# Optimization experiments

Measured on AMD Instinct MI355X. Metric: run time of the kernel, lower is better.

The kernel has to match this reference:

```python
import jax, jax.numpy as jnp
import numpy as np

DIM = 512
HEADS = 8
R = 8  # reduction_ratio
EPS = 1e-08


def setup_inputs() -> dict:
    key = jax.random.key(0)
    k1, k2, k3, k4, k5 = jax.random.split(key, 5)
    B, H, W = 2, 128, 128
    x = jax.random.normal(k1, (B, DIM, H, W), dtype=jnp.float32)
    mask = jax.random.uniform(k2, (B, 1, H, W), dtype=jnp.float32)
    # learned params (conv weights, OIHW)
    Wq = jax.random.normal(k3, (DIM, DIM, 1, 1), dtype=jnp.float32) * 0.02
    Wkv = jax.random.normal(k4, (2 * DIM, DIM, R, R), dtype=jnp.float32) * 0.02
    Wo = jax.random.normal(k5, (DIM, DIM, 1, 1), dtype=jnp.float32) * 0.02
    return {"x": x, "mask": mask, "Wq": Wq, "Wkv": Wkv, "Wo": Wo}


def reference(x, mask, Wq, Wkv, Wo):
    B, C, H, W = x.shape
    heads = HEADS
    hd = C // heads  # head dim
    scale = hd ** (-0.5)
    N = H * W
    Hr, Wr = H // R, W // R
    L = Hr * Wr

    # to_q: 1x1 conv (no bias)
    q = jnp.einsum('bchw,oc->bohw', x, Wq[:, :, 0, 0])
    # to_kv: conv kernel R stride R (no bias)
    kv = jax.lax.conv_general_dilated(
        x, Wkv, window_strides=(R, R), padding='VALID',
        dimension_numbers=('NCHW', 'OIHW', 'NCHW'))
    k, v = jnp.split(kv, 2, axis=1)  # each [B, C, Hr, Wr]

    # nn.Unfold(R, stride=R) on [B,1,H,W] then mean over patch dim == avg-pool R/R
    mask_down = mask.reshape(B, Hr, R, Wr, R).mean(axis=(2, 4)).reshape(B, L)  # [B, L]
    m_flat = mask.reshape(B, N)  # [B, N]  (c == 1)
    # rank-1 outer-product bias, then log
    bias = jnp.log(m_flat[:, :, None] * mask_down[:, None, :] + EPS)  # [B, N, L]

    def to_tokens(t, n):
        # 'b (h c) x y -> (b h) (x y) c'
        Bt = t.shape[0]
        return t.reshape(Bt, heads, hd, n).transpose(0, 1, 3, 2).reshape(Bt * heads, n, hd)

    qh = to_tokens(q, N)   # [B*heads, N, hd]
    kh = to_tokens(k, L)   # [B*heads, L, hd]
    vh = to_tokens(v, L)   # [B*heads, L, hd]

    # torch mask.repeat(heads,1,1): tiles whole [B,...] block heads times -> index i uses bias[i % B]
    bias_rep = jnp.tile(bias, (heads, 1, 1))  # [heads*B, N, L]

    sim = (jnp.einsum('bic,bjc->bij', qh, kh) + bias_rep) * scale
    attn = jax.nn.softmax(sim, axis=-1)
    out = jnp.einsum('bij,bjc->bic', attn, vh)  # [B*heads, N, hd]

    # '(b h) (x y) c -> b (h c) x y'
    out = out.reshape(B, heads, N, hd).transpose(0, 1, 3, 2).reshape(B, C, H, W)
    return jnp.einsum('bchw,oc->bohw', out, Wo[:, :, 0, 0])
```

## Files before the change

kernel.cpp:

```cpp
#include <hip/hip_runtime.h>
#include <math.h>

#define DIMC  512
#define HEADS 8
#define HD    64
#define NPIX  16384
#define LTOK  256
#define BATCH 2
#define WIMG  128
#define KVK   32768
#define EPSB  1e-8f
#define SCALEF 0.125f
#define SPLITK 16
#define KCHUNK (KVK / SPLITK)

typedef unsigned short ushort_t;
typedef unsigned int uint_t;
using bf16x8 = __attribute__((ext_vector_type(8))) __bf16;
using f32x4  = __attribute__((ext_vector_type(4))) float;

__device__ __forceinline__ ushort_t f2bf(float f) {
    union { float f; unsigned u; } v; v.f = f;
    unsigned r = v.u + 0x7FFFu + ((v.u >> 16) & 1u);
    return (ushort_t)(r >> 16);
}
__device__ __forceinline__ float bf2f(ushort_t h) {
    union { unsigned u; float f; } v; v.u = ((unsigned)h) << 16;
    return v.f;
}
__device__ __forceinline__ uint_t pk2bf(float a, float b) {
    return (uint_t)f2bf(a) | ((uint_t)f2bf(b) << 16);
}
__device__ __forceinline__ void gl16(const void* g, void* l) {
    __builtin_amdgcn_global_load_lds(
        (const __attribute__((address_space(1))) unsigned int*)g,
        (__attribute__((address_space(3))) unsigned int*)l, 16, 0, 0);
}

__global__ void k_maskdown(const float* __restrict__ mask, float* __restrict__ md) {
    int b = blockIdx.x;
    int l = threadIdx.x;
    int hr = l >> 4, wr = l & 15;
    const float* mp = mask + (size_t)b * NPIX;
    float s = 0.f;
#pragma unroll
    for (int i = 0; i < 8; ++i)
#pragma unroll
        for (int j = 0; j < 8; ++j)
            s += mp[(hr * 8 + i) * WIMG + wr * 8 + j];
    md[b * LTOK + l] = s * (1.f / 64.f);
}

__global__ __launch_bounds__(256) void k_xt(const float* __restrict__ x, ushort_t* __restrict__ xt) {
    __shared__ float t[64][65];
    int b = blockIdx.z, c0 = blockIdx.y * 64, n0 = blockIdx.x * 64;
    int tn = threadIdx.x & 63, tc = threadIdx.x >> 6;
    const float* xb = x + ((size_t)b * DIMC + c0) * NPIX + n0;
#pragma unroll
    for (int p = 0; p < 16; ++p)
        t[tc + p * 4][tn] = xb[(size_t)(tc + p * 4) * NPIX + tn];
    __syncthreads();
    ushort_t* xtb = xt + ((size_t)b * NPIX + n0) * DIMC + c0;
#pragma unroll
    for (int p = 0; p < 16; ++p) {
        int nl = tc + p * 4;
        xtb[(size_t)nl * DIMC + tn] = f2bf(t[tn][nl]);
    }
}

__global__ __launch_bounds__(256) void k_wkvp(const float* __restrict__ Wkv, ushort_t* __restrict__ Wp) {
    __shared__ float t[64][65];
    int o = blockIdx.y, c0 = blockIdx.x * 64;
    int tij = threadIdx.x & 63, tc = threadIdx.x >> 6;
    const float* wb = Wkv + ((size_t)o * DIMC + c0) * 64;
#pragma unroll
    for (int p = 0; p < 16; ++p)
        t[tc + p * 4][tij] = wb[(size_t)(tc + p * 4) * 64 + tij];
    __syncthreads();
    ushort_t* wpb = Wp + (size_t)o * KVK + c0;
#pragma unroll
    for (int p = 0; p < 16; ++p) {
        int ij = tc + p * 4;
        wpb[(size_t)ij * DIMC + tij] = f2bf(t[tij][ij]);
    }
}

__global__ void k_cvt(const float* __restrict__ s, ushort_t* __restrict__ d) {
    int i = blockIdx.x * 256 + threadIdx.x;
    d[i] = f2bf(s[i]);
}

template<int EPI>
__global__ __launch_bounds__(256) void k_gemm_qo(
    const ushort_t* __restrict__ A, long sA,
    const ushort_t* __restrict__ B, long sB,
    void* __restrict__ Yv) {
    __shared__ ushort_t Asm[2][128 * 64];
    __shared__ ushort_t Bsm[2][128 * 64];
    const int tid = threadIdx.x;
    const int w = tid >> 6, lane = tid & 63;
    const int wm = w >> 1, wn = w & 1;
    const int lr = lane & 15, lg = lane >> 4;
    const int bz = blockIdx.z;
    const int m0 = blockIdx.y * 128, c0 = blockIdx.x * 128;
    const ushort_t* Ab = A + (size_t)bz * sA;
    const ushort_t* Bb = B + (size_t)bz * sB;

    f32x4 acc[4][4];
    const f32x4 zz = {0.f, 0.f, 0.f, 0.f};
#pragma unroll
    for (int i = 0; i < 4; ++i)
#pragma unroll
        for (int j = 0; j < 4; ++j) acc[i][j] = zz;

#define STAGE_QO(buf, k0) do {                                               \
    _Pragma("unroll")                                                        \
    for (int r = 0; r < 4; ++r) {                                            \
        int slot = r * 256 + tid;                                            \
        int m = slot >> 3, kb = slot & 7;                                    \
        int kbs = kb ^ (m & 7);                                              \
        gl16(Ab + (size_t)(m0 + m) * DIMC + (k0) + kbs * 8,                  \
             &Asm[buf][(size_t)(r * 256 + w * 64) * 8]);                     \
    }                                                                        \
    _Pragma("unroll")                                                        \
    for (int r = 0; r < 4; ++r) {                                            \
        int slot = r * 256 + tid;                                            \
        int m = slot >> 3, kb = slot & 7;                                    \
        int kbs = kb ^ (m & 7);                                              \
        gl16(Bb + (size_t)(c0 + m) * DIMC + (k0) + kbs * 8,                  \
             &Bsm[buf][(size_t)(r * 256 + w * 64) * 8]);                     \
    }                                                                        \
} while (0)

    STAGE_QO(0, 0);
    __syncthreads();
    int cur = 0;
#pragma unroll 1
    for (int t = 0; t < 8; ++t) {
        if (t < 7) STAGE_QO(cur ^ 1, (t + 1) * 64);
#pragma unroll
        for (int kk = 0; kk < 2; ++kk) {
            bf16x8 af[4], bfr[4];
#pragma unroll
            for (int i = 0; i < 4; ++i) {
                int row = wm * 64 + i * 16 + lr;
                af[i] = *(const bf16x8*)&Asm[cur][(size_t)(row * 8 + ((kk * 4 + lg) ^ (row & 7))) * 8];
            }
#pragma unroll
            for (int j = 0; j < 4; ++j) {
                int row = wn * 64 + j * 16 + lr;
                bfr[j] = *(const bf16x8*)&Bsm[cur][(size_t)(row * 8 + ((kk * 4 + lg) ^ (row & 7))) * 8];
            }
#pragma unroll
            for (int i = 0; i < 4; ++i)
#pragma unroll
                for (int j = 0; j < 4; ++j)
                    acc[i][j] = __builtin_amdgcn_mfma_f32_16x16x32_bf16(af[i], bfr[j], acc[i][j], 0, 0, 0);
        }
        if (t < 7) {
            __syncthreads();
            cur ^= 1;
        }
    }
#undef STAGE_QO

    if (EPI == 0) {
        ushort_t* q = (ushort_t*)Yv + (size_t)bz * ((size_t)NPIX * DIMC);
#pragma unroll
        for (int i = 0; i < 4; ++i) {
            int d0 = m0 + wm * 64 + i * 16 + lg * 4;
#pragma unroll
            for (int j = 0; j < 4; ++j) {
                int n = c0 + wn * 64 + j * 16 + lr;
                ushort4 v;
                v.x = f2bf(acc[i][j][0]); v.y = f2bf(acc[i][j][1]);
                v.z = f2bf(acc[i][j][2]); v.w = f2bf(acc[i][j][3]);
                *(ushort4*)&q[(size_t)n * DIMC + d0] = v;
            }
        }
    } else {
        float* O = (float*)Yv + (size_t)bz * ((size_t)DIMC * NPIX);
#pragma unroll
        for (int i = 0; i < 4; ++i) {
            int n0r = m0 + wm * 64 + i * 16 + lg * 4;
#pragma unroll
            for (int j = 0; j < 4; ++j) {
                int o = c0 + wn * 64 + j * 16 + lr;
                *(f32x4*)&O[(size_t)o * NPIX + n0r] = acc[i][j];
            }
        }
    }
}

__global__ __launch_bounds__(256) void k_convkv_mfma(
    const ushort_t* __restrict__ xt, const ushort_t* __restrict__ Wp,
    float* __restrict__ part) {
    __shared__ ushort_t Asm[2][128 * 64];
    __shared__ ushort_t Bsm[2][128 * 64];
    const int tid = threadIdx.x;
    const int w = tid >> 6, lane = tid & 63;
    const int wm = w >> 1, wn = w & 1;
    const int lr = lane & 15, lg = lane >> 4;
    const int z = blockIdx.z;
    const int b = z >> 4, ks = z & 15;
    const int m0 = blockIdx.y * 128, n0 = blockIdx.x * 128;
    const ushort_t* xtb = xt + (size_t)b * NPIX * DIMC;
    const int kbeg = ks * KCHUNK;

    f32x4 acc[4][4];
    const f32x4 zz = {0.f, 0.f, 0.f, 0.f};
#pragma unroll
    for (int i = 0; i < 4; ++i)
#pragma unroll
        for (int j = 0; j < 4; ++j) acc[i][j] = zz;

#define STAGE_KV(buf, k0) do {                                               \
    _Pragma("unroll")                                                        \
    for (int r = 0; r < 4; ++r) {                                            \
        int slot = r * 256 + tid;                                            \
        int m = slot >> 3, kb = slot & 7;                                    \
        int kbs = kb ^ (m & 7);                                              \
        gl16(Wp + (size_t)(m0 + m) * KVK + (k0) + kbs * 8,                   \
             &Asm[buf][(size_t)(r * 256 + w * 64) * 8]);                     \
    }                                                                        \
    _Pragma("unroll")                                                        \
    for (int r = 0; r < 4; ++r) {                                            \
        int slot = r * 256 + tid;                                            \
        int nn = slot >> 3, kb = slot & 7;                                   \
        int l = n0 + nn, hr = l >> 4, wr = l & 15;                           \
        int kp = (k0) + (kb ^ (nn & 7)) * 8;                                 \
        int ij = kp >> 9, ck = kp & 511;                                     \
        int ii = ij >> 3, jj = ij & 7;                                       \
        gl16(xtb + (size_t)((hr * 8 + ii) * WIMG + wr * 8 + jj) * DIMC + ck, \
             &Bsm[buf][(size_t)(r * 256 + w * 64) * 8]);                     \
    }                                                                        \
} while (0)

    STAGE_KV(0, kbeg);
    __syncthreads();
    int cur = 0;
#pragma unroll 1
    for (int t = 0; t < KCHUNK / 64; ++t) {
        if (t < KCHUNK / 64 - 1) STAGE_KV(cur ^ 1, kbeg + (t + 1) * 64);
#pragma unroll
        for (int kk = 0; kk < 2; ++kk) {
            bf16x8 af[4], bfr[4];
#pragma unroll
            for (int i = 0; i < 4; ++i) {
                int row = wm * 64 + i * 16 + lr;
                af[i] = *(const bf16x8*)&Asm[cur][(size_t)(row * 8 + ((kk * 4 + lg) ^ (row & 7))) * 8];
            }
#pragma unroll
            for (int j = 0; j < 4; ++j) {
                int row = wn * 64 + j * 16 + lr;
                bfr[j] = *(const bf16x8*)&Bsm[cur][(size_t)(row * 8 + ((kk * 4 + lg) ^ (row & 7))) * 8];
            }
#pragma unroll
            for (int i = 0; i < 4; ++i)
#pragma unroll
                for (int j = 0; j < 4; ++j)
                    acc[i][j] = __builtin_amdgcn_mfma_f32_16x16x32_bf16(af[i], bfr[j], acc[i][j], 0, 0, 0);
        }
        if (t < KCHUNK / 64 - 1) {
            __syncthreads();
            cur ^= 1;
        }
    }
#undef STAGE_KV

    float* P = part + (size_t)z * (LTOK * 1024);
#pragma unroll
    for (int i = 0; i < 4; ++i) {
        int o0 = m0 + wm * 64 + i * 16 + lg * 4;
#pragma unroll
        for (int j = 0; j < 4; ++j) {
            int l = n0 + wn * 64 + j * 16 + lr;
            *(f32x4*)&P[(size_t)l * 1024 + o0] = acc[i][j];
        }
    }
}

__global__ void k_kvreduce(const float* __restrict__ part,
                           ushort_t* __restrict__ kt, ushort_t* __restrict__ vt) {
    int idx = blockIdx.x * 256 + threadIdx.x;
    int o = idx & 1023;
    int rest = idx >> 10;
    int l = rest & 255, b = rest >> 8;
    float s = 0.f;
#pragma unroll
    for (int ks = 0; ks < SPLITK; ++ks)
        s += part[(size_t)(b * SPLITK + ks) * (LTOK * 1024) + (size_t)l * 1024 + o];
    int h = (o >> 6) & 7, d = o & 63;
    if (o < 512)
        kt[(((size_t)b * 8 + h) * 256 + l) * 64 + d] = f2bf(s);
    else
        vt[(((size_t)b * 8 + h) * 64 + d) * 256 + l] = f2bf(s);
}

__global__ __launch_bounds__(256, 2) void k_attn_mfma(
    const ushort_t* __restrict__ qbf, const ushort_t* __restrict__ kt,
    const ushort_t* __restrict__ vt, const float* __restrict__ mask,
    const float* __restrict__ md, ushort_t* __restrict__ obuf) {
    __shared__ ushort_t Qs[128 * 64];
    __shared__ ushort_t Ks[256 * 64];
    __shared__ ushort_t Vs[64 * 256];

    const int tid = threadIdx.x;
    const int w = tid >> 6, lane = tid & 63;
    const int g = lane >> 4, ln = lane & 15;
    const int bh = blockIdx.y, b = bh >> 3, h = bh & 7;
    const int bb = bh & 1;
    const int n0 = blockIdx.x * 128;

    {
        const ushort_t* src = qbf + ((size_t)b * NPIX + n0) * DIMC + h * 64;
#pragma unroll
        for (int p = 0; p < 4; ++p) {
            int id = p * 256 + tid;
            int r = id >> 3, s = id & 7;
            uint4 v = *(const uint4*)(src + (size_t)r * DIMC + s * 8);
            *(uint4*)&Qs[(r * 8 + (s ^ (r & 7))) * 8] = v;
        }
    }
    {
        const ushort_t* src = kt + (size_t)bh * 256 * 64;
#pragma unroll
        for (int p = 0; p < 8; ++p) {
            int id = p * 256 + tid;
            int r = id >> 3, s = id & 7;
            uint4 v = *(const uint4*)(src + r * 64 + s * 8);
            *(uint4*)&Ks[(r * 8 + (s ^ (r & 7))) * 8] = v;
        }
    }
    {
        const ushort_t* src = vt + (size_t)bh * 64 * 256;
#pragma unroll
        for (int p = 0; p < 8; ++p) {
            int id = p * 256 + tid;
            int r = id >> 5, s = id & 31;
            uint4 v = *(const uint4*)(src + r * 256 + s * 8);
            *(uint4*)&Vs[(r * 32 + (s ^ (r & 7))) * 8] = v;
        }
    }
    __syncthreads();

    f32x4 acc[2][16];
    const f32x4 zz = {0.f, 0.f, 0.f, 0.f};
#pragma unroll
    for (int nf = 0; nf < 2; ++nf)
#pragma unroll
        for (int f = 0; f < 16; ++f) acc[nf][f] = zz;

    bf16x8 qf[2][2];
#pragma unroll
    for (int nf = 0; nf < 2; ++nf)
#pragma unroll
        for (int kk = 0; kk < 2; ++kk) {
            int nl = 32 * w + nf * 16 + ln;
            qf[nf][kk] = *(const bf16x8*)&Qs[(nl * 8 + ((kk * 4 + g) ^ (nl & 7))) * 8];
        }
#pragma unroll
    for (int f = 0; f < 16; ++f) {
#pragma unroll
        for (int kk = 0; kk < 2; ++kk) {
            int l = f * 16 + ln;
            bf16x8 kf = *(const bf16x8*)&Ks[(l * 8 + ((kk * 4 + g) ^ (l & 7))) * 8];
            acc[0][f] = __builtin_amdgcn_mfma_f32_16x16x32_bf16(kf, qf[0][kk], acc[0][f], 0, 0, 0);
            acc[1][f] = __builtin_amdgcn_mfma_f32_16x16x32_bf16(kf, qf[1][kk], acc[1][f], 0, 0, 0);
        }
    }

    float inv[2];
    uint2 pb[2][16];
#pragma unroll
    for (int nf = 0; nf < 2; ++nf) {
        float mval = mask[(size_t)bb * NPIX + n0 + 32 * w + nf * 16 + ln];
        float mx = -1e30f;
#pragma unroll
        for (int f = 0; f < 16; ++f) {
            float4 md4 = *(const float4*)&md[bb * LTOK + f * 16 + g * 4];
            float s0 = (acc[nf][f][0] + __logf(mval * md4.x + EPSB)) * SCALEF;
            float s1 = (acc[nf][f][1] + __logf(mval * md4.y + EPSB)) * SCALEF;
            float s2 = (acc[nf][f][2] + __logf(mval * md4.z + EPSB)) * SCALEF;
            float s3 = (acc[nf][f][3] + __logf(mval * md4.w + EPSB)) * SCALEF;
            acc[nf][f][0] = s0; acc[nf][f][1] = s1;
            acc[nf][f][2] = s2; acc[nf][f][3] = s3;
            mx = fmaxf(mx, fmaxf(fmaxf(s0, s1), fmaxf(s2, s3)));
        }
        mx = fmaxf(mx, __shfl_xor(mx, 16));
        mx = fmaxf(mx, __shfl_xor(mx, 32));
        float sum = 0.f;
#pragma unroll
        for (int f = 0; f < 16; ++f) {
            float p0 = __expf(acc[nf][f][0] - mx);
            float p1 = __expf(acc[nf][f][1] - mx);
            float p2 = __expf(acc[nf][f][2] - mx);
            float p3 = __expf(acc[nf][f][3] - mx);
            sum += (p0 + p1) + (p2 + p3);
            pb[nf][f].x = pk2bf(p0, p1);
            pb[nf][f].y = pk2bf(p2, p3);
        }
        sum += __shfl_xor(sum, 16);
        sum += __shfl_xor(sum, 32);
        inv[nf] = 1.f / sum;
    }

    f32x4 acc2[2][4];
#pragma unroll
    for (int nf = 0; nf < 2; ++nf)
#pragma unroll
        for (int df = 0; df < 4; ++df) acc2[nf][df] = zz;

    const int srcLo = ((g & 1) << 5) + ln;
    const bool selHi = (g >> 1);
#pragma unroll
    for (int ks = 0; ks < 8; ++ks) {
        bf16x8 vf[4];
#pragma unroll
        for (int df = 0; df < 4; ++df) {
            int d = df * 16 + ln;
            vf[df] = *(const bf16x8*)&Vs[(d * 32 + ((ks * 4 + g) ^ (d & 7))) * 8];
        }
#pragma unroll
        for (int nf = 0; nf < 2; ++nf) {
            uint_t e0 = pb[nf][2 * ks].x,     e1 = pb[nf][2 * ks].y;
            uint_t o0 = pb[nf][2 * ks + 1].x, o1 = pb[nf][2 * ks + 1].y;
            uint_t lo0 = __shfl((int)e0, srcLo), lo1 = __shfl((int)e1, srcLo);
            uint_t lo0b = __shfl((int)o0, srcLo), lo1b = __shfl((int)o1, srcLo);
            uint_t hi0 = __shfl((int)e0, srcLo + 16), hi1 = __shfl((int)e1, srcLo + 16);
            uint_t hi0b = __shfl((int)o0, srcLo + 16), hi1b = __shfl((int)o1, srcLo + 16);
            union { uint_t u[4]; bf16x8 v; } bfr;
            bfr.u[0] = selHi ? lo0b : lo0;
            bfr.u[1] = selHi ? lo1b : lo1;
            bfr.u[2] = selHi ? hi0b : hi0;
            bfr.u[3] = selHi ? hi1b : hi1;
#pragma unroll
            for (int df = 0; df < 4; ++df)
                acc2[nf][df] = __builtin_amdgcn_mfma_f32_16x16x32_bf16(vf[df], bfr.v, acc2[nf][df], 0, 0, 0);
        }
    }

#pragma unroll
    for (int nf = 0; nf < 2; ++nf) {
        int n = n0 + 32 * w + nf * 16 + ln;
        ushort_t* op = obuf + ((size_t)b * NPIX + n) * DIMC + h * 64;
#pragma unroll
        for (int df = 0; df < 4; ++df) {
            ushort4 v;
            v.x = f2bf(acc2[nf][df][0] * inv[nf]);
            v.y = f2bf(acc2[nf][df][1] * inv[nf]);
            v.z = f2bf(acc2[nf][df][2] * inv[nf]);
            v.w = f2bf(acc2[nf][df][3] * inv[nf]);
            *(ushort4*)&op[df * 16 + g * 4] = v;
        }
    }
}

extern "C" void kernel_launch(void* const* d_in, const int* in_sizes, int n_in,
                              void* d_out, int out_size, void* d_ws, size_t ws_size,
                              hipStream_t stream) {
    const float* x    = (const float*)d_in[0];
    const float* mask = (const float*)d_in[1];
    const float* Wq   = (const float*)d_in[2];
    const float* Wkv  = (const float*)d_in[3];
    const float* Wo   = (const float*)d_in[4];
    float* out = (float*)d_out;

    char* ws = (char*)d_ws;
    float*    md   = (float*)(ws);
    ushort_t* xt   = (ushort_t*)(ws + 4096);
    ushort_t* wkvp = (ushort_t*)(ws + 33558528);
    ushort_t* qbf  = wkvp;
    ushort_t* ktb  = (ushort_t*)(ws + 100667392);
    ushort_t* vtb  = ktb + 524288;
    ushort_t* wqb  = (ushort_t*)(ws + 102764544);
    ushort_t* wob  = wqb + 262144;
    float*    part = (float*)(ws + 103813120);
    ushort_t* aob  = (ushort_t*)part;

    k_maskdown<<<dim3(BATCH), dim3(256), 0, stream>>>(mask, md);
    k_xt<<<dim3(NPIX / 64, DIMC / 64, BATCH), dim3(256), 0, stream>>>(x, xt);
    k_cvt<<<dim3(1024), dim3(256), 0, stream>>>(Wq, wqb);
    k_cvt<<<dim3(1024), dim3(256), 0, stream>>>(Wo, wob);
    k_wkvp<<<dim3(DIMC / 64, 1024), dim3(256), 0, stream>>>(Wkv, wkvp);

    k_convkv_mfma<<<dim3(LTOK / 128, 1024 / 128, BATCH * SPLITK), dim3(256), 0, stream>>>(xt, wkvp, part);
    k_kvreduce<<<dim3(2048), dim3(256), 0, stream>>>(part, ktb, vtb);

    k_gemm_qo<0><<<dim3(NPIX / 128, DIMC / 128, BATCH), dim3(256), 0, stream>>>(
        wqb, 0L, xt, (long)NPIX * DIMC, qbf);

    k_attn_mfma<<<dim3(NPIX / 128, BATCH * HEADS), dim3(256), 0, stream>>>(
        qbf, ktb, vtb, mask, md, aob);

    k_gemm_qo<1><<<dim3(DIMC / 128, NPIX / 128, BATCH), dim3(256), 0, stream>>>(
        aob, (long)NPIX * DIMC, wob, 0L, out);
}
```

Measured before the change: 248.3 us.

## Fuse Q projection into attention kernel and remap convkv blocks across XCDs

```diff
diff --git a/kernel.cpp b/kernel.cpp
--- a/kernel.cpp
+++ b/kernel.cpp
@@ -90,11 +90,10 @@
     d[i] = f2bf(s[i]);
 }
 
-template<int EPI>
-__global__ __launch_bounds__(256) void k_gemm_qo(
+__global__ __launch_bounds__(256) void k_gemm_o(
     const ushort_t* __restrict__ A, long sA,
     const ushort_t* __restrict__ B, long sB,
-    void* __restrict__ Yv) {
+    float* __restrict__ Yv) {
     __shared__ ushort_t Asm[2][128 * 64];
     __shared__ ushort_t Bsm[2][128 * 64];
     const int tid = threadIdx.x;
@@ -164,30 +163,14 @@
     }
 #undef STAGE_QO
 
-    if (EPI == 0) {
-        ushort_t* q = (ushort_t*)Yv + (size_t)bz * ((size_t)NPIX * DIMC);
-#pragma unroll
-        for (int i = 0; i < 4; ++i) {
-            int d0 = m0 + wm * 64 + i * 16 + lg * 4;
-#pragma unroll
-            for (int j = 0; j < 4; ++j) {
-                int n = c0 + wn * 64 + j * 16 + lr;
-                ushort4 v;
-                v.x = f2bf(acc[i][j][0]); v.y = f2bf(acc[i][j][1]);
-                v.z = f2bf(acc[i][j][2]); v.w = f2bf(acc[i][j][3]);
-                *(ushort4*)&q[(size_t)n * DIMC + d0] = v;
-            }
-        }
-    } else {
-        float* O = (float*)Yv + (size_t)bz * ((size_t)DIMC * NPIX);
-#pragma unroll
-        for (int i = 0; i < 4; ++i) {
-            int n0r = m0 + wm * 64 + i * 16 + lg * 4;
-#pragma unroll
-            for (int j = 0; j < 4; ++j) {
-                int o = c0 + wn * 64 + j * 16 + lr;
-                *(f32x4*)&O[(size_t)o * NPIX + n0r] = acc[i][j];
-            }
+    float* O = Yv + (size_t)bz * ((size_t)DIMC * NPIX);
+#pragma unroll
+    for (int i = 0; i < 4; ++i) {
+        int n0r = m0 + wm * 64 + i * 16 + lg * 4;
+#pragma unroll
+        for (int j = 0; j < 4; ++j) {
+            int o = c0 + wn * 64 + j * 16 + lr;
+            *(f32x4*)&O[(size_t)o * NPIX + n0r] = acc[i][j];
         }
     }
 }
@@ -201,9 +184,12 @@
     const int w = tid >> 6, lane = tid & 63;
     const int wm = w >> 1, wn = w & 1;
     const int lr = lane & 15, lg = lane >> 4;
-    const int z = blockIdx.z;
+    const int f = blockIdx.x;
+    const int xcd = f & 7, idx = f >> 3;
+    const int z = (idx >> 4) * 8 + xcd;
+    const int inner = idx & 15;
+    const int m0 = (inner >> 1) * 128, n0 = (inner & 1) * 128;
     const int b = z >> 4, ks = z & 15;
-    const int m0 = blockIdx.y * 128, n0 = blockIdx.x * 128;
     const ushort_t* xtb = xt + (size_t)b * NPIX * DIMC;
     const int kbeg = ks * KCHUNK;
 
@@ -298,10 +284,10 @@
 }
 
 __global__ __launch_bounds__(256, 2) void k_attn_mfma(
-    const ushort_t* __restrict__ qbf, const ushort_t* __restrict__ kt,
-    const ushort_t* __restrict__ vt, const float* __restrict__ mask,
-    const float* __restrict__ md, ushort_t* __restrict__ obuf) {
-    __shared__ ushort_t Qs[128 * 64];
+    const ushort_t* __restrict__ xt, const ushort_t* __restrict__ wqb,
+    const ushort_t* __restrict__ kt, const ushort_t* __restrict__ vt,
+    const float* __restrict__ mask, const float* __restrict__ md,
+    ushort_t* __restrict__ obuf) {
     __shared__ ushort_t Ks[256 * 64];
     __shared__ ushort_t Vs[64 * 256];
 
@@ -313,16 +299,6 @@
     const int n0 = blockIdx.x * 128;
 
     {
-        const ushort_t* src = qbf + ((size_t)b * NPIX + n0) * DIMC + h * 64;
-#pragma unroll
-        for (int p = 0; p < 4; ++p) {
-            int id = p * 256 + tid;
-            int r = id >> 3, s = id & 7;
-            uint4 v = *(const uint4*)(src + (size_t)r * DIMC + s * 8);
-            *(uint4*)&Qs[(r * 8 + (s ^ (r & 7))) * 8] = v;
-        }
-    }
-    {
         const ushort_t* src = kt + (size_t)bh * 256 * 64;
 #pragma unroll
         for (int p = 0; p < 8; ++p) {
@@ -342,23 +318,74 @@
             *(uint4*)&Vs[(r * 32 + (s ^ (r & 7))) * 8] = v;
         }
     }
+
+    f32x4 aq[4][2];
+    const f32x4 zz = {0.f, 0.f, 0.f, 0.f};
+#pragma unroll
+    for (int i = 0; i < 4; ++i)
+#pragma unroll
+        for (int nf = 0; nf < 2; ++nf) aq[i][nf] = zz;
+    {
+        const ushort_t* wq0 = wqb + (size_t)(h * 64 + ln) * DIMC;
+        const ushort_t* xr0 = xt + ((size_t)b * NPIX + n0 + 32 * w + ln) * DIMC;
+#pragma unroll
+        for (int kc = 0; kc < 16; ++kc) {
+            int off = kc * 32 + 8 * g;
+            bf16x8 af[4], bq[2];
+#pragma unroll
+            for (int i = 0; i < 4; ++i)
+                af[i] = *(const bf16x8*)(wq0 + (size_t)(16 * i) * DIMC + off);
+#pragma unroll
+            for (int nf = 0; nf < 2; ++nf)
+                bq[nf] = *(const bf16x8*)(xr0 + (size_t)(16 * nf) * DIMC + off);
+#pragma unroll
+            for (int i = 0; i < 4; ++i)
+#pragma unroll
+                for (int nf = 0; nf < 2; ++nf)
+                    aq[i][nf] = __builtin_amdgcn_mfma_f32_16x16x32_bf16(af[i], bq[nf], aq[i][nf], 0, 0, 0);
+        }
+    }
+    bf16x8 qf[2][2];
+    {
+        uint_t uq[4][2][2];
+#pragma unroll
+        for (int i = 0; i < 4; ++i)
+#pragma unroll
+            for (int nf = 0; nf < 2; ++nf) {
+                uq[i][nf][0] = pk2bf(aq[i][nf][0], aq[i][nf][1]);
+                uq[i][nf][1] = pk2bf(aq[i][nf][2], aq[i][nf][3]);
+            }
+        const int srcA = (((2 * g) & 3) << 4) + ln;
+        const int srcB = (((2 * g + 1) & 3) << 4) + ln;
+        const bool hi = (g >> 1);
+#pragma unroll
+        for (int nf = 0; nf < 2; ++nf)
+#pragma unroll
+            for (int kk = 0; kk < 2; ++kk) {
+                uint_t w0l = __shfl((int)uq[2 * kk][nf][0], srcA);
+                uint_t w0h = __shfl((int)uq[2 * kk + 1][nf][0], srcA);
+                uint_t w1l = __shfl((int)uq[2 * kk][nf][1], srcA);
+                uint_t w1h = __shfl((int)uq[2 * kk + 1][nf][1], srcA);
+                uint_t w2l = __shfl((int)uq[2 * kk][nf][0], srcB);
+                uint_t w2h = __shfl((int)uq[2 * kk + 1][nf][0], srcB);
+                uint_t w3l = __shfl((int)uq[2 * kk][nf][1], srcB);
+                uint_t w3h = __shfl((int)uq[2 * kk + 1][nf][1], srcB);
+                union { uint_t u[4]; bf16x8 v; } t;
+                t.u[0] = hi ? w0h : w0l;
+                t.u[1] = hi ? w1h : w1l;
+                t.u[2] = hi ? w2h : w2l;
+                t.u[3] = hi ? w3h : w3l;
+                qf[nf][kk] = t.v;
+            }
+    }
     __syncthreads();
 
     f32x4 acc[2][16];
-    const f32x4 zz = {0.f, 0.f, 0.f, 0.f};
 #pragma unroll
     for (int nf = 0; nf < 2; ++nf)
 #pragma unroll
         for (int f = 0; f < 16; ++f) acc[nf][f] = zz;
 
-    bf16x8 qf[2][2];
-#pragma unroll
-    for (int nf = 0; nf < 2; ++nf)
-#pragma unroll
-        for (int kk = 0; kk < 2; ++kk) {
-            int nl = 32 * w + nf * 16 + ln;
-            qf[nf][kk] = *(const bf16x8*)&Qs[(nl * 8 + ((kk * 4 + g) ^ (nl & 7))) * 8];
-        }
 #pragma unroll
     for (int f = 0; f < 16; ++f) {
 #pragma unroll
@@ -470,7 +497,6 @@
     float*    md   = (float*)(ws);
     ushort_t* xt   = (ushort_t*)(ws + 4096);
     ushort_t* wkvp = (ushort_t*)(ws + 33558528);
-    ushort_t* qbf  = wkvp;
     ushort_t* ktb  = (ushort_t*)(ws + 100667392);
     ushort_t* vtb  = ktb + 524288;
     ushort_t* wqb  = (ushort_t*)(ws + 102764544);
@@ -484,15 +510,12 @@
     k_cvt<<<dim3(1024), dim3(256), 0, stream>>>(Wo, wob);
     k_wkvp<<<dim3(DIMC / 64, 1024), dim3(256), 0, stream>>>(Wkv, wkvp);
 
-    k_convkv_mfma<<<dim3(LTOK / 128, 1024 / 128, BATCH * SPLITK), dim3(256), 0, stream>>>(xt, wkvp, part);
+    k_convkv_mfma<<<dim3(512), dim3(256), 0, stream>>>(xt, wkvp, part);
     k_kvreduce<<<dim3(2048), dim3(256), 0, stream>>>(part, ktb, vtb);
 
-    k_gemm_qo<0><<<dim3(NPIX / 128, DIMC / 128, BATCH), dim3(256), 0, stream>>>(
-        wqb, 0L, xt, (long)NPIX * DIMC, qbf);
-
     k_attn_mfma<<<dim3(NPIX / 128, BATCH * HEADS), dim3(256), 0, stream>>>(
-        qbf, ktb, vtb, mask, md, aob);
-
-    k_gemm_qo<1><<<dim3(DIMC / 128, NPIX / 128, BATCH), dim3(256), 0, stream>>>(
+        xt, wqb, ktb, vtb, mask, md, aob);
+
+    k_gemm_o<<<dim3(DIMC / 128, NPIX / 128, BATCH), dim3(256), 0, stream>>>(
         aob, (long)NPIX * DIMC, wob, 0L, out);
 }
```

Result: slower. 289.3 us (+16.5%).

## Vectorize transpose stores, merge weight converts, remap convkv blocks per XCD

Applied to the files above, without the earlier changes.

```diff
diff --git a/kernel.cpp b/kernel.cpp
--- a/kernel.cpp
+++ b/kernel.cpp
@@ -24,10 +24,6 @@
     unsigned r = v.u + 0x7FFFu + ((v.u >> 16) & 1u);
     return (ushort_t)(r >> 16);
 }
-__device__ __forceinline__ float bf2f(ushort_t h) {
-    union { unsigned u; float f; } v; v.u = ((unsigned)h) << 16;
-    return v.f;
-}
 __device__ __forceinline__ uint_t pk2bf(float a, float b) {
     return (uint_t)f2bf(a) | ((uint_t)f2bf(b) << 16);
 }
@@ -61,10 +57,16 @@
         t[tc + p * 4][tn] = xb[(size_t)(tc + p * 4) * NPIX + tn];
     __syncthreads();
     ushort_t* xtb = xt + ((size_t)b * NPIX + n0) * DIMC + c0;
-#pragma unroll
-    for (int p = 0; p < 16; ++p) {
-        int nl = tc + p * 4;
-        xtb[(size_t)nl * DIMC + tn] = f2bf(t[tn][nl]);
+    int tc4 = threadIdx.x & 15, ng = threadIdx.x >> 4;
+#pragma unroll
+    for (int p = 0; p < 4; ++p) {
+        int nl = ng + p * 16;
+        ushort4 v;
+        v.x = f2bf(t[4 * tc4 + 0][nl]);
+        v.y = f2bf(t[4 * tc4 + 1][nl]);
+        v.z = f2bf(t[4 * tc4 + 2][nl]);
+        v.w = f2bf(t[4 * tc4 + 3][nl]);
+        *(ushort4*)&xtb[(size_t)nl * DIMC + 4 * tc4] = v;
     }
 }
 
@@ -78,16 +80,24 @@
         t[tc + p * 4][tij] = wb[(size_t)(tc + p * 4) * 64 + tij];
     __syncthreads();
     ushort_t* wpb = Wp + (size_t)o * KVK + c0;
-#pragma unroll
-    for (int p = 0; p < 16; ++p) {
-        int ij = tc + p * 4;
-        wpb[(size_t)ij * DIMC + tij] = f2bf(t[tij][ij]);
-    }
-}
-
-__global__ void k_cvt(const float* __restrict__ s, ushort_t* __restrict__ d) {
+    int tj4 = threadIdx.x & 15, ig = threadIdx.x >> 4;
+#pragma unroll
+    for (int p = 0; p < 4; ++p) {
+        int ij = ig + p * 16;
+        ushort4 v;
+        v.x = f2bf(t[4 * tj4 + 0][ij]);
+        v.y = f2bf(t[4 * tj4 + 1][ij]);
+        v.z = f2bf(t[4 * tj4 + 2][ij]);
+        v.w = f2bf(t[4 * tj4 + 3][ij]);
+        *(ushort4*)&wpb[(size_t)ij * DIMC + 4 * tj4] = v;
+    }
+}
+
+__global__ void k_cvt2(const float* __restrict__ a, const float* __restrict__ b,
+                       ushort_t* __restrict__ da, ushort_t* __restrict__ db) {
     int i = blockIdx.x * 256 + threadIdx.x;
-    d[i] = f2bf(s[i]);
+    if (i < 262144) da[i] = f2bf(a[i]);
+    else            db[i - 262144] = f2bf(b[i - 262144]);
 }
 
 template<int EPI>
@@ -201,9 +211,12 @@
     const int w = tid >> 6, lane = tid & 63;
     const int wm = w >> 1, wn = w & 1;
     const int lr = lane & 15, lg = lane >> 4;
-    const int z = blockIdx.z;
+    const int f = blockIdx.x;
+    const int xcd = f & 7, idx = f >> 3;
+    const int z = (idx >> 4) * 8 + xcd;
+    const int inner = idx & 15;
+    const int m0 = (inner >> 1) * 128, n0 = (inner & 1) * 128;
     const int b = z >> 4, ks = z & 15;
-    const int m0 = blockIdx.y * 128, n0 = blockIdx.x * 128;
     const ushort_t* xtb = xt + (size_t)b * NPIX * DIMC;
     const int kbeg = ks * KCHUNK;
 
@@ -480,11 +493,10 @@
 
     k_maskdown<<<dim3(BATCH), dim3(256), 0, stream>>>(mask, md);
     k_xt<<<dim3(NPIX / 64, DIMC / 64, BATCH), dim3(256), 0, stream>>>(x, xt);
-    k_cvt<<<dim3(1024), dim3(256), 0, stream>>>(Wq, wqb);
-    k_cvt<<<dim3(1024), dim3(256), 0, stream>>>(Wo, wob);
+    k_cvt2<<<dim3(2048), dim3(256), 0, stream>>>(Wq, Wo, wqb, wob);
     k_wkvp<<<dim3(DIMC / 64, 1024), dim3(256), 0, stream>>>(Wkv, wkvp);
 
-    k_convkv_mfma<<<dim3(LTOK / 128, 1024 / 128, BATCH * SPLITK), dim3(256), 0, stream>>>(xt, wkvp, part);
+    k_convkv_mfma<<<dim3(512), dim3(256), 0, stream>>>(xt, wkvp, part);
     k_kvreduce<<<dim3(2048), dim3(256), 0, stream>>>(part, ktb, vtb);
 
     k_gemm_qo<0><<<dim3(NPIX / 128, DIMC / 128, BATCH), dim3(256), 0, stream>>>(
```

After: 255.3 us. 2.8% more time.
